# Kernel optimization log

Measured on AMD Instinct MI355X. Metric: run time of the kernel, lower is better.

## Reference

```python
import jax, jax.numpy as jnp
import numpy as np

DELTA = 10.0


def setup_inputs() -> dict:
    key = jax.random.key(0)
    k1, k2 = jax.random.split(key)
    B = 8192
    pred = jax.random.normal(k1, (B,), dtype=jnp.float32)
    target = jax.random.randint(k2, (B,), 0, 2, dtype=jnp.int64)
    return {"pred": pred, "target": target}


def reference(pred, target):
    pred = jnp.squeeze(pred)
    t = jnp.squeeze(target)
    # pairwise delta: D[i, j] = pred[i] - pred[j]
    D = pred[:, None] - pred[None, :]
    m01 = (t[:, None] == 0) & (t[None, :] == 1)  # (neg, pos) pair
    m10 = (t[:, None] == 1) & (t[None, :] == 0)  # (pos, neg) pair
    h01 = jnp.square(jnp.maximum(DELTA - D, 0.0))
    h10 = jnp.square(jnp.maximum(DELTA + D, 0.0))
    loss_sum = jnp.sum(jnp.where(m01, h01, 0.0)) + jnp.sum(jnp.where(m10, h10, 0.0))
    N = (jnp.sum(m01) + jnp.sum(m10)).astype(jnp.float32)
    # T counts correctly-ordered pairs: pred[pos] > pred[neg]
    T = (jnp.sum(m01 & (D < 0.0)) + jnp.sum(m10 & (D > 0.0))).astype(jnp.float32)
    return loss_sum / N, T / N
```

## Files before the change

### kernel.cpp

```cpp
#include <hip/hip_runtime.h>

#define TJ 256
#define II 4
#define DELTA 10.0f

__global__ void __launch_bounds__(256)
pair_kernel(const float* __restrict__ pred, const int* __restrict__ target,
            int B, int nTj,
            unsigned* __restrict__ tc_part, float* __restrict__ corr_part) {
    __shared__ float vsh[TJ];
    __shared__ float wsh[TJ];
    __shared__ float smaxs[4];
    __shared__ unsigned stc[4];
    __shared__ float scr[4];

    const int tid = threadIdx.x;
    const int bi = blockIdx.x / nTj;
    const int bj = blockIdx.x % nTj;

    const int jg = bj * TJ + tid;
    float vj = 1e30f, wj = -1e30f;
    if (jg < B && target[jg] == 0) { const float y = pred[jg]; vj = y; wj = y; }
    vsh[tid] = vj;
    wsh[tid] = wj;

    float wmax = wj;
    #pragma unroll
    for (int off = 32; off > 0; off >>= 1)
        wmax = fmaxf(wmax, __shfl_xor(wmax, off));
    if ((tid & 63) == 0) smaxs[tid >> 6] = wmax;
    __syncthreads();
    const float tileMax = fmaxf(fmaxf(smaxs[0], smaxs[1]),
                                fmaxf(smaxs[2], smaxs[3]));

    float u[II], xx[II];
    float xmin = 1e30f;
    #pragma unroll
    for (int k = 0; k < II; ++k) {
        u[k] = -1e30f; xx[k] = 1e30f;
        const int ig = bi * (II * 256) + k * 256 + tid;
        if (ig < B && target[ig] == 1) {
            const float x = pred[ig];
            u[k] = x; xx[k] = DELTA + x;
        }
        xmin = fminf(xmin, xx[k]);
    }

    unsigned tc = 0;
    float corr = 0.0f;
    const float4* v4 = (const float4*)vsh;
    if (__all(xmin >= tileMax)) {
        #pragma unroll 8
        for (int jj = 0; jj < TJ / 4; ++jj) {
            const float4 vv = v4[jj];
            #pragma unroll
            for (int k = 0; k < II; ++k) {
                tc += (u[k] > vv.x);
                tc += (u[k] > vv.y);
                tc += (u[k] > vv.z);
                tc += (u[k] > vv.w);
            }
        }
    } else {
        const float4* w4 = (const float4*)wsh;
        #pragma unroll 4
        for (int jj = 0; jj < TJ / 4; ++jj) {
            const float4 vv = v4[jj];
            const float4 ww = w4[jj];
            #pragma unroll
            for (int k = 0; k < II; ++k) {
                float dm;
                tc += (u[k] > vv.x); dm = fminf(xx[k] - ww.x, 0.0f); corr = fmaf(dm, dm, corr);
                tc += (u[k] > vv.y); dm = fminf(xx[k] - ww.y, 0.0f); corr = fmaf(dm, dm, corr);
                tc += (u[k] > vv.z); dm = fminf(xx[k] - ww.z, 0.0f); corr = fmaf(dm, dm, corr);
                tc += (u[k] > vv.w); dm = fminf(xx[k] - ww.w, 0.0f); corr = fmaf(dm, dm, corr);
            }
        }
    }

    #pragma unroll
    for (int off = 32; off > 0; off >>= 1) {
        tc += __shfl_xor(tc, off);
        corr += __shfl_xor(corr, off);
    }
    if ((tid & 63) == 0) { stc[tid >> 6] = tc; scr[tid >> 6] = corr; }
    __syncthreads();
    if (tid == 0) {
        tc_part[blockIdx.x]   = stc[0] + stc[1] + stc[2] + stc[3];
        corr_part[blockIdx.x] = scr[0] + scr[1] + scr[2] + scr[3];
    }
}

__global__ void __launch_bounds__(1024)
finalize_kernel(const float* __restrict__ pred, const int* __restrict__ target,
                int B, const unsigned* __restrict__ tc_part,
                const float* __restrict__ corr_part, int nParts,
                float* __restrict__ out) {
    __shared__ double sred[16][8];
    __shared__ double fin[8];
    const int tid = threadIdx.x;

    double tc = 0.0, corr = 0.0;
    for (int k = tid; k < nParts; k += 1024) {
        tc   += (double)tc_part[k];
        corr += (double)corr_part[k];
    }

    double a1 = 0, a2 = 0, s1 = 0, s2 = 0, P = 0, Nn = 0;
    const float4* p4 = (const float4*)pred;
    const int4*   t4 = (const int4*)target;
    for (int i = tid; i < B / 4; i += 1024) {
        const float4 pv = p4[i];
        const int4   tv = t4[i];
        const float px[4] = {pv.x, pv.y, pv.z, pv.w};
        const int   tx[4] = {tv.x, tv.y, tv.z, tv.w};
        #pragma unroll
        for (int k = 0; k < 4; ++k) {
            const double x = (double)px[k];
            if (tx[k] == 1) { const double z = 10.0 + x; a1 += z; a2 += z * z; P += 1.0; }
            else if (tx[k] == 0) { s1 += x; s2 += x * x; Nn += 1.0; }
        }
    }

    double q[8] = {tc, corr, a1, a2, s1, s2, P, Nn};
    #pragma unroll
    for (int off = 32; off > 0; off >>= 1) {
        #pragma unroll
        for (int a = 0; a < 8; ++a) q[a] += __shfl_xor(q[a], off);
    }
    if ((tid & 63) == 0) {
        #pragma unroll
        for (int a = 0; a < 8; ++a) sred[tid >> 6][a] = q[a];
    }
    __syncthreads();
    if (tid < 8) {
        double s = 0.0;
        #pragma unroll
        for (int w = 0; w < 16; ++w) s += sred[w][tid];
        fin[tid] = s;
    }
    __syncthreads();
    if (tid == 0) {
        const double Pc = fin[6], Nc = fin[7];
        const double lossSum = Nc * fin[3] - 2.0 * fin[2] * fin[4]
                             + Pc * fin[5] - fin[1];
        const double Np = Pc * Nc;
        out[0] = (float)(lossSum / Np);
        out[1] = (float)(fin[0] / Np);
    }
}

extern "C" void kernel_launch(void* const* d_in, const int* in_sizes, int n_in,
                              void* d_out, int out_size, void* d_ws, size_t ws_size,
                              hipStream_t stream) {
    const float* pred = (const float*)d_in[0];
    const int* target = (const int*)d_in[1];
    const int B = in_sizes[0];

    const int nTi = (B + II * 256 - 1) / (II * 256);
    const int nTj = (B + TJ - 1) / TJ;
    const int nb = nTi * nTj;

    unsigned* tc_part = (unsigned*)d_ws;
    float* corr_part  = (float*)((char*)d_ws + (((size_t)nb * 4 + 255) & ~(size_t)255));

    pair_kernel<<<nb, 256, 0, stream>>>(pred, target, B, nTj, tc_part, corr_part);
    finalize_kernel<<<1, 1024, 0, stream>>>(pred, target, B, tc_part, corr_part,
                                            nb, (float*)d_out);
}
```

Before: 19.17 us.

## Fuse finalize into pair kernel via atomics and compact negative tiles

Result: slower. 20.57 us (+7.3%).

```diff
diff --git a/kernel.cpp b/kernel.cpp
--- a/kernel.cpp
+++ b/kernel.cpp
@@ -5,33 +5,56 @@
 #define DELTA 10.0f
 
 __global__ void __launch_bounds__(256)
-pair_kernel(const float* __restrict__ pred, const int* __restrict__ target,
-            int B, int nTj,
-            unsigned* __restrict__ tc_part, float* __restrict__ corr_part) {
+fused_kernel(const float* __restrict__ pred, const int* __restrict__ target,
+             int B, int nTj, int nb,
+             double* __restrict__ acc, unsigned* __restrict__ ticket,
+             float* __restrict__ out) {
     __shared__ float vsh[TJ];
     __shared__ float wsh[TJ];
+    __shared__ int   swtot[4];
     __shared__ float smaxs[4];
-    __shared__ unsigned stc[4];
-    __shared__ float scr[4];
+    __shared__ double sred[4][8];
+    __shared__ double facc[8];
+    __shared__ unsigned s_last;
 
     const int tid = threadIdx.x;
+    const int lane = tid & 63;
+    const int wv = tid >> 6;
     const int bi = blockIdx.x / nTj;
     const int bj = blockIdx.x % nTj;
 
     const int jg = bj * TJ + tid;
-    float vj = 1e30f, wj = -1e30f;
-    if (jg < B && target[jg] == 0) { const float y = pred[jg]; vj = y; wj = y; }
-    vsh[tid] = vj;
-    wsh[tid] = wj;
+    float y = 0.0f; int t = -1;
+    if (jg < B) { y = pred[jg]; t = target[jg]; }
+    const bool isneg = (t == 0);
 
-    float wmax = wj;
+    double a1 = 0, a2 = 0, s1 = 0, s2 = 0, Pc = 0, Nc = 0;
+    if (bi == 0) {
+        if (t == 1) { const double z = 10.0 + (double)y; a1 = z; a2 = z * z; Pc = 1.0; }
+        else if (isneg) { const double yd = (double)y; s1 = yd; s2 = yd * yd; Nc = 1.0; }
+    }
+
+    const unsigned long long m = __ballot(isneg);
+    const unsigned long long lm = (1ull << lane) - 1ull;
+    const int ppre = __popcll(m & lm);
+    if (lane == 0) swtot[wv] = __popcll(m);
+    float wmax = isneg ? y : -1e30f;
     #pragma unroll
     for (int off = 32; off > 0; off >>= 1)
         wmax = fmaxf(wmax, __shfl_xor(wmax, off));
-    if ((tid & 63) == 0) smaxs[tid >> 6] = wmax;
+    if (lane == 0) smaxs[wv] = wmax;
     __syncthreads();
+
+    int base = 0;
+    #pragma unroll
+    for (int w = 0; w < 4; ++w) base += (w < wv) ? swtot[w] : 0;
+    const int nneg = swtot[0] + swtot[1] + swtot[2] + swtot[3];
+    const int npad = (nneg + 3) & ~3;
     const float tileMax = fmaxf(fmaxf(smaxs[0], smaxs[1]),
                                 fmaxf(smaxs[2], smaxs[3]));
+    if (isneg) { vsh[base + ppre] = y; wsh[base + ppre] = y; }
+    if (tid < npad - nneg) { vsh[nneg + tid] = 1e30f; wsh[nneg + tid] = -1e30f; }
+    __syncthreads();
 
     float u[II], xx[II];
     float xmin = 1e30f;
@@ -48,10 +71,11 @@
 
     unsigned tc = 0;
     float corr = 0.0f;
+    const int nj4 = npad >> 2;
     const float4* v4 = (const float4*)vsh;
     if (__all(xmin >= tileMax)) {
-        #pragma unroll 8
-        for (int jj = 0; jj < TJ / 4; ++jj) {
+        #pragma unroll 4
+        for (int jj = 0; jj < nj4; ++jj) {
             const float4 vv = v4[jj];
             #pragma unroll
             for (int k = 0; k < II; ++k) {
@@ -63,8 +87,8 @@
         }
     } else {
         const float4* w4 = (const float4*)wsh;
-        #pragma unroll 4
-        for (int jj = 0; jj < TJ / 4; ++jj) {
+        #pragma unroll 2
+        for (int jj = 0; jj < nj4; ++jj) {
             const float4 vv = v4[jj];
             const float4 ww = w4[jj];
             #pragma unroll
@@ -78,75 +102,40 @@
         }
     }
 
-    #pragma unroll
-    for (int off = 32; off > 0; off >>= 1) {
-        tc += __shfl_xor(tc, off);
-        corr += __shfl_xor(corr, off);
-    }
-    if ((tid & 63) == 0) { stc[tid >> 6] = tc; scr[tid >> 6] = corr; }
-    __syncthreads();
-    if (tid == 0) {
-        tc_part[blockIdx.x]   = stc[0] + stc[1] + stc[2] + stc[3];
-        corr_part[blockIdx.x] = scr[0] + scr[1] + scr[2] + scr[3];
-    }
-}
-
-__global__ void __launch_bounds__(1024)
-finalize_kernel(const float* __restrict__ pred, const int* __restrict__ target,
-                int B, const unsigned* __restrict__ tc_part,
-                const float* __restrict__ corr_part, int nParts,
-                float* __restrict__ out) {
-    __shared__ double sred[16][8];
-    __shared__ double fin[8];
-    const int tid = threadIdx.x;
-
-    double tc = 0.0, corr = 0.0;
-    for (int k = tid; k < nParts; k += 1024) {
-        tc   += (double)tc_part[k];
-        corr += (double)corr_part[k];
-    }
-
-    double a1 = 0, a2 = 0, s1 = 0, s2 = 0, P = 0, Nn = 0;
-    const float4* p4 = (const float4*)pred;
-    const int4*   t4 = (const int4*)target;
-    for (int i = tid; i < B / 4; i += 1024) {
-        const float4 pv = p4[i];
-        const int4   tv = t4[i];
-        const float px[4] = {pv.x, pv.y, pv.z, pv.w};
-        const int   tx[4] = {tv.x, tv.y, tv.z, tv.w};
-        #pragma unroll
-        for (int k = 0; k < 4; ++k) {
-            const double x = (double)px[k];
-            if (tx[k] == 1) { const double z = 10.0 + x; a1 += z; a2 += z * z; P += 1.0; }
-            else if (tx[k] == 0) { s1 += x; s2 += x * x; Nn += 1.0; }
-        }
-    }
-
-    double q[8] = {tc, corr, a1, a2, s1, s2, P, Nn};
+    double q[8] = {(double)tc, (double)corr, a1, a2, s1, s2, Pc, Nc};
     #pragma unroll
     for (int off = 32; off > 0; off >>= 1) {
         #pragma unroll
         for (int a = 0; a < 8; ++a) q[a] += __shfl_xor(q[a], off);
     }
-    if ((tid & 63) == 0) {
+    if (lane == 0) {
         #pragma unroll
-        for (int a = 0; a < 8; ++a) sred[tid >> 6][a] = q[a];
+        for (int a = 0; a < 8; ++a) sred[wv][a] = q[a];
     }
     __syncthreads();
+
     if (tid < 8) {
-        double s = 0.0;
-        #pragma unroll
-        for (int w = 0; w < 16; ++w) s += sred[w][tid];
-        fin[tid] = s;
+        const double tot = sred[0][tid] + sred[1][tid] + sred[2][tid] + sred[3][tid];
+        atomicAdd(&acc[tid], tot);
+    }
+    asm volatile("s_waitcnt vmcnt(0)" ::: "memory");
+    if (tid == 0) {
+        const unsigned old = atomicAdd(ticket, 1u);
+        s_last = (old == (unsigned)(nb - 1)) ? 1u : 0u;
     }
     __syncthreads();
-    if (tid == 0) {
-        const double Pc = fin[6], Nc = fin[7];
-        const double lossSum = Nc * fin[3] - 2.0 * fin[2] * fin[4]
-                             + Pc * fin[5] - fin[1];
-        const double Np = Pc * Nc;
-        out[0] = (float)(lossSum / Np);
-        out[1] = (float)(fin[0] / Np);
+
+    if (s_last) {
+        if (tid < 8) facc[tid] = atomicAdd(&acc[tid], 0.0);
+        __syncthreads();
+        if (tid == 0) {
+            const double P = facc[6], Nn = facc[7];
+            const double lossSum = Nn * facc[3] - 2.0 * facc[2] * facc[4]
+                                 + P * facc[5] - facc[1];
+            const double Np = P * Nn;
+            out[0] = (float)(lossSum / Np);
+            out[1] = (float)(facc[0] / Np);
+        }
     }
 }
 
@@ -161,10 +150,10 @@
     const int nTj = (B + TJ - 1) / TJ;
     const int nb = nTi * nTj;
 
-    unsigned* tc_part = (unsigned*)d_ws;
-    float* corr_part  = (float*)((char*)d_ws + (((size_t)nb * 4 + 255) & ~(size_t)255));
+    double* acc      = (double*)d_ws;
+    unsigned* ticket = (unsigned*)((char*)d_ws + 64);
 
-    pair_kernel<<<nb, 256, 0, stream>>>(pred, target, B, nTj, tc_part, corr_part);
-    finalize_kernel<<<1, 1024, 0, stream>>>(pred, target, B, tc_part, corr_part,
-                                            nb, (float*)d_out);
+    hipMemsetAsync(d_ws, 0, 128, stream);
+    fused_kernel<<<nb, 256, 0, stream>>>(pred, target, B, nTj, nb,
+                                         acc, ticket, (float*)d_out);
 }
```
